# Kernel tuning notes

Hardware: AMD Instinct MI355X
Metric: run time of the kernel (lower is better)

The kernel has to match this reference:

```python
import jax, jax.numpy as jnp
from jax import lax
import numpy as np

DN = ('NCHW', 'OIHW', 'NCHW')

def conv_reflect(x, w, b, pad):
    # torch Conv2d with padding_mode='reflect': reflect-pad then valid conv
    x = jnp.pad(x, ((0, 0), (0, 0), (pad, pad), (pad, pad)), mode='reflect')
    y = lax.conv_general_dilated(x, w, (1, 1), 'VALID', dimension_numbers=DN)
    return y + b[None, :, None, None]

def setup_inputs() -> dict:
    key = jax.random.key(0)
    ks = jax.random.split(key, 8)
    B, W, H = 4, 1024, 1024
    inp = {
        'input': jax.random.normal(ks[0], (B, 12, W, H), dtype=jnp.float32),
        'w1': jax.random.normal(ks[1], (32, 12, 7, 7), dtype=jnp.float32) * 0.05,
        'b1': jnp.zeros((32,), dtype=jnp.float32),
        'w2': jax.random.normal(ks[2], (32, 32, 5, 5), dtype=jnp.float32) * 0.05,
        'b2': jnp.zeros((32,), dtype=jnp.float32),
        'w3': jax.random.normal(ks[3], (8, 32, 5, 5), dtype=jnp.float32) * 0.05,
        'b3': jnp.zeros((8,), dtype=jnp.float32),
        'dwkernel': jax.random.normal(ks[4], (8, 1, 7, 7), dtype=jnp.float32),
    }
    return inp

def reference(input, w1, b1, w2, b2, w3, b3, dwkernel):
    B, _, W, H = input.shape
    color = input[:, 0:3]
    albedo = input[:, 3:6]
    albedo = jnp.where(albedo < 0.001, jnp.float32(1.0), albedo)
    color = color / albedo
    net_in = jnp.concatenate([color, albedo, input[:, 6:]], axis=1)  # (B,12,W,H)

    h = jax.nn.relu(conv_reflect(net_in, w1, b1, 3))
    h = jax.nn.relu(conv_reflect(h, w2, b2, 2))
    logits = conv_reflect(h, w3, b3, 2)  # (B,8,W,H)
    kernel = jax.nn.softmax(logits / 5.0, axis=1)  # (B,8,W,H)

    # grouped conv: dwkernel repeated over 3 color channels, zero padding=3
    rpk = jnp.tile(dwkernel, (3, 1, 1, 1))  # (24,1,7,7)
    preconv = lax.conv_general_dilated(
        color, rpk, (1, 1), [(3, 3), (3, 3)],
        dimension_numbers=DN, feature_group_count=3,
    )  # (B,24,W,H)
    preconv = preconv.reshape(B, 3, 8, W, H)

    # (kernel expanded over color dim * preconv).sum over kernel dim
    filtered = jnp.einsum('bkwh,bckwh->bcwh', kernel, preconv)
    remodulated = albedo * filtered
    return remodulated
```

## Files before the change

kernel.cpp:

```cpp
#include <hip/hip_runtime.h>

#define IMG 1024

typedef _Float16 half8 __attribute__((ext_vector_type(8)));
typedef float f32x4 __attribute__((ext_vector_type(4)));

__device__ __forceinline__ int refl(int i) {
    i = (i < 0) ? -i : i;
    return (i >= IMG) ? (2 * IMG - 2 - i) : i;
}
__device__ __forceinline__ float afix(float a) { return (a < 0.001f) ? 1.0f : a; }
__device__ __forceinline__ int iclamp(int v, int lo, int hi) { return v < lo ? lo : (v > hi ? hi : v); }
__device__ __forceinline__ int swz64(int a) { return a ^ (((((a >> 6) & 3) ^ ((a >> 8) & 1)) << 4)); }
__device__ __forceinline__ int swz32(int a) { return a ^ ((((a >> 7) & 1)) << 4); }
__device__ __forceinline__ unsigned short h2b(_Float16 h) { union { _Float16 f; unsigned short u; } x; x.f = h; return x.u; }

__global__ void wprep_kernel(const float* __restrict__ w1, const float* __restrict__ w2,
                             const float* __restrict__ w3,
                             char* __restrict__ w1p, char* __restrict__ w2p, char* __restrict__ w3p)
{
    const int NF1 = 7 * 2 * 4 * 2, NF2 = 5 * 2 * 5 * 2, NF3 = 5 * 5 * 2;
    int gid = blockIdx.x * 256 + threadIdx.x;
    int f = gid >> 6, l = gid & 63;
    if (f >= NF1 + NF2 + NF3) return;
    int r = l & 15, g = l >> 4;
    half8 out;
    char* dst;
    if (f < NF1) {
        int pl = f & 1, j = (f >> 1) & 3, oct = (f >> 3) & 1, ky = f >> 4;
        int oc = oct * 16 + r;
#pragma unroll
        for (int e = 0; e < 8; e++) {
            int k = g * 8 + e, kx = 2 * j + (k >> 4), ic = k & 15;
            float v = (ic < 12 && kx < 7) ? w1[((oc * 12 + ic) * 7 + ky) * 7 + kx] : 0.f;
            _Float16 h = (_Float16)v;
            out[e] = pl ? (_Float16)(v - (float)h) : h;
        }
        dst = w1p + (size_t)f * 1024 + l * 16;
    } else if (f < NF1 + NF2) {
        int ff = f - NF1;
        int pl = ff & 1, t2 = ff >> 1;
        int kx = t2 % 5; t2 /= 5;
        int oct = t2 & 1, ky = t2 >> 1;
        int oc = oct * 16 + r;
#pragma unroll
        for (int e = 0; e < 8; e++) {
            int ic = g * 8 + e;
            float v = w2[((oc * 32 + ic) * 5 + ky) * 5 + kx];
            _Float16 h = (_Float16)v;
            out[e] = pl ? (_Float16)(v - (float)h) : h;
        }
        dst = w2p + (size_t)ff * 1024 + l * 16;
    } else {
        int ff = f - NF1 - NF2;
        int pl = ff & 1, t2 = ff >> 1;
        int kx = t2 % 5, ky = t2 / 5;
#pragma unroll
        for (int e = 0; e < 8; e++) {
            int ic = g * 8 + e;
            float v = (r < 8) ? w3[((r * 32 + ic) * 5 + ky) * 5 + kx] : 0.f;
            _Float16 h = (_Float16)v;
            out[e] = pl ? (_Float16)(v - (float)h) : h;
        }
        dst = w3p + (size_t)ff * 1024 + l * 16;
    }
    *(half8*)dst = out;
}

__global__ void netin_kernel(const float* __restrict__ in, char* __restrict__ nh, char* __restrict__ nl)
{
    const int M = IMG * IMG;
    int px = blockIdx.x * 256 + threadIdx.x;
    float v[16];
#pragma unroll
    for (int c = 0; c < 3; c++) {
        float a = afix(in[(size_t)(c + 3) * M + px]);
        v[c] = (in[(size_t)c * M + px] / a) * 0.25f;
        v[c + 3] = a * 0.25f;
    }
#pragma unroll
    for (int c = 6; c < 12; c++) v[c] = in[(size_t)c * M + px] * 0.25f;
#pragma unroll
    for (int c = 12; c < 16; c++) v[c] = 0.f;
    unsigned short hb[16], lb[16];
#pragma unroll
    for (int c = 0; c < 16; c++) {
        _Float16 h = (_Float16)v[c];
        hb[c] = h2b(h);
        lb[c] = h2b((_Float16)(v[c] - (float)h));
    }
    *(int4*)(nh + (size_t)px * 32) = *(int4*)&hb[0];
    *(int4*)(nh + (size_t)px * 32 + 16) = *(int4*)&hb[8];
    *(int4*)(nl + (size_t)px * 32) = *(int4*)&lb[0];
    *(int4*)(nl + (size_t)px * 32 + 16) = *(int4*)&lb[8];
}

__global__ __launch_bounds__(256, 4) void conv1_mfma(
    const char* __restrict__ nh, const char* __restrict__ nl,
    const char* __restrict__ w1p, const float* __restrict__ b1,
    char* __restrict__ h1h, char* __restrict__ h1l, int a1, int e1)
{
    __shared__ __align__(16) char sm[14 * 1280];
    const int t = threadIdx.x, l = t & 63, w = t >> 6;
    const int c = l & 15, g = l >> 4;
    const int x0 = blockIdx.x * 32;
    const int ystart = a1 + blockIdx.y * 8;
    const int pxt = w & 1, rbase = (w >> 1) * 4;

    f32x4 zero4 = {0.f, 0.f, 0.f, 0.f};
    f32x4 acc[2][4];
#pragma unroll
    for (int o = 0; o < 2; o++)
#pragma unroll
        for (int r = 0; r < 4; r++) acc[o][r] = zero4;

    for (int q = t; q < 1120; q += 256) {
        int slab = q / 80, c2 = q % 80;
        int px = c2 >> 1, s = c2 & 1;
        int gy = refl(ystart + slab - 3);
        int gx = refl(x0 + px - 3);
        *(int4*)(sm + slab * 1280 + swz32(px * 32 + s * 16)) =
            *(const int4*)(nh + ((size_t)gy * IMG + gx) * 32 + s * 16);
    }
    __syncthreads();
#pragma unroll 1
    for (int ky = 0; ky < 7; ky++) {
        half8 aw0[2][4], aw1[2][4];
#pragma unroll
        for (int oct = 0; oct < 2; oct++)
#pragma unroll
            for (int j = 0; j < 4; j++) {
                aw0[oct][j] = *(const half8*)(w1p + (size_t)((((ky * 2 + oct) * 4 + j) * 2 + 0)) * 1024 + l * 16);
                aw1[oct][j] = *(const half8*)(w1p + (size_t)((((ky * 2 + oct) * 4 + j) * 2 + 1)) * 1024 + l * 16);
            }
#pragma unroll
        for (int r = 0; r < 4; r++) {
            const char* base = sm + (rbase + r + ky) * 1280;
#pragma unroll
            for (int j = 0; j < 4; j++) {
                int p2 = pxt * 16 + c + 2 * j + (g >> 1);
                half8 bh = *(const half8*)(base + swz32(p2 * 32 + (g & 1) * 16));
#pragma unroll
                for (int oct = 0; oct < 2; oct++) {
                    acc[oct][r] = __builtin_amdgcn_mfma_f32_16x16x32_f16(aw0[oct][j], bh, acc[oct][r], 0, 0, 0);
                    acc[oct][r] = __builtin_amdgcn_mfma_f32_16x16x32_f16(aw1[oct][j], bh, acc[oct][r], 0, 0, 0);
                }
            }
        }
    }
    __syncthreads();
    for (int q = t; q < 1120; q += 256) {
        int slab = q / 80, c2 = q % 80;
        int px = c2 >> 1, s = c2 & 1;
        int gy = refl(ystart + slab - 3);
        int gx = refl(x0 + px - 3);
        *(int4*)(sm + slab * 1280 + swz32(px * 32 + s * 16)) =
            *(const int4*)(nl + ((size_t)gy * IMG + gx) * 32 + s * 16);
    }
    __syncthreads();
#pragma unroll 1
    for (int ky = 0; ky < 7; ky++) {
        half8 aw0[2][4];
#pragma unroll
        for (int oct = 0; oct < 2; oct++)
#pragma unroll
            for (int j = 0; j < 4; j++)
                aw0[oct][j] = *(const half8*)(w1p + (size_t)((((ky * 2 + oct) * 4 + j) * 2 + 0)) * 1024 + l * 16);
#pragma unroll
        for (int r = 0; r < 4; r++) {
            const char* base = sm + (rbase + r + ky) * 1280;
#pragma unroll
            for (int j = 0; j < 4; j++) {
                int p2 = pxt * 16 + c + 2 * j + (g >> 1);
                half8 bl = *(const half8*)(base + swz32(p2 * 32 + (g & 1) * 16));
#pragma unroll
                for (int oct = 0; oct < 2; oct++)
                    acc[oct][r] = __builtin_amdgcn_mfma_f32_16x16x32_f16(aw0[oct][j], bl, acc[oct][r], 0, 0, 0);
            }
        }
    }
#pragma unroll
    for (int r = 0; r < 4; r++) {
        int y = ystart + rbase + r;
        if (y < e1) {
            int x = x0 + pxt * 16 + c, ybuf = y - a1;
#pragma unroll
            for (int oct = 0; oct < 2; oct++) {
                ushort4 hv, lv;
                float vv[4];
#pragma unroll
                for (int i = 0; i < 4; i++) {
                    int oc = oct * 16 + g * 4 + i;
                    float v = acc[oct][r][i] * 4.f + b1[oc];
                    vv[i] = fmaxf(v, 0.f) * 0.125f;
                }
                _Float16 h0 = (_Float16)vv[0], h1_ = (_Float16)vv[1], h2_ = (_Float16)vv[2], h3 = (_Float16)vv[3];
                hv.x = h2b(h0); hv.y = h2b(h1_); hv.z = h2b(h2_); hv.w = h2b(h3);
                lv.x = h2b((_Float16)(vv[0] - (float)h0)); lv.y = h2b((_Float16)(vv[1] - (float)h1_));
                lv.z = h2b((_Float16)(vv[2] - (float)h2_)); lv.w = h2b((_Float16)(vv[3] - (float)h3));
                size_t ob = ((size_t)ybuf * IMG + x) * 64 + oct * 32 + g * 8;
                *(ushort4*)(h1h + ob) = hv;
                *(ushort4*)(h1l + ob) = lv;
            }
        }
    }
}

__global__ __launch_bounds__(256, 4) void conv2_mfma(
    const char* __restrict__ h1h, const char* __restrict__ h1l,
    const char* __restrict__ w2p, const float* __restrict__ b2,
    char* __restrict__ h2h, char* __restrict__ h2l,
    int a1, int e1, int a2, int e2)
{
    __shared__ __align__(16) char sm[12 * 2304];
    const int t = threadIdx.x, l = t & 63, w = t >> 6;
    const int c = l & 15, g = l >> 4;
    const int x0 = blockIdx.x * 32;
    const int ystart = a2 + blockIdx.y * 8;
    const int pxt = w & 1, rbase = (w >> 1) * 4;

    f32x4 zero4 = {0.f, 0.f, 0.f, 0.f};
    f32x4 acc[2][4];
#pragma unroll
    for (int o = 0; o < 2; o++)
#pragma unroll
        for (int r = 0; r < 4; r++) acc[o][r] = zero4;

    for (int q = t; q < 1728; q += 256) {
        int slab = q / 144, c2 = q % 144;
        int px = c2 >> 2, s = c2 & 3;
        int yy = iclamp(refl(ystart + slab - 2), a1, e1 - 1) - a1;
        int gx = refl(x0 + px - 2);
        *(int4*)(sm + slab * 2304 + swz64(px * 64 + s * 16)) =
            *(const int4*)(h1h + ((size_t)yy * IMG + gx) * 64 + s * 16);
    }
    __syncthreads();
#pragma unroll 1
    for (int ky = 0; ky < 5; ky++) {
        half8 aw0[2][5], aw1[2][5];
#pragma unroll
        for (int oct = 0; oct < 2; oct++)
#pragma unroll
            for (int kx = 0; kx < 5; kx++) {
                aw0[oct][kx] = *(const half8*)(w2p + (size_t)((((ky * 2 + oct) * 5 + kx) * 2 + 0)) * 1024 + l * 16);
                aw1[oct][kx] = *(const half8*)(w2p + (size_t)((((ky * 2 + oct) * 5 + kx) * 2 + 1)) * 1024 + l * 16);
            }
#pragma unroll
        for (int r = 0; r < 4; r++) {
            const char* base = sm + (rbase + r + ky) * 2304;
#pragma unroll
            for (int kx = 0; kx < 5; kx++) {
                half8 bh = *(const half8*)(base + swz64((pxt * 16 + c + kx) * 64 + g * 16));
#pragma unroll
                for (int oct = 0; oct < 2; oct++) {
                    acc[oct][r] = __builtin_amdgcn_mfma_f32_16x16x32_f16(aw0[oct][kx], bh, acc[oct][r], 0, 0, 0);
                    acc[oct][r] = __builtin_amdgcn_mfma_f32_16x16x32_f16(aw1[oct][kx], bh, acc[oct][r], 0, 0, 0);
                }
            }
        }
    }
    __syncthreads();
    for (int q = t; q < 1728; q += 256) {
        int slab = q / 144, c2 = q % 144;
        int px = c2 >> 2, s = c2 & 3;
        int yy = iclamp(refl(ystart + slab - 2), a1, e1 - 1) - a1;
        int gx = refl(x0 + px - 2);
        *(int4*)(sm + slab * 2304 + swz64(px * 64 + s * 16)) =
            *(const int4*)(h1l + ((size_t)yy * IMG + gx) * 64 + s * 16);
    }
    __syncthreads();
#pragma unroll 1
    for (int ky = 0; ky < 5; ky++) {
        half8 aw0[2][5];
#pragma unroll
        for (int oct = 0; oct < 2; oct++)
#pragma unroll
            for (int kx = 0; kx < 5; kx++)
                aw0[oct][kx] = *(const half8*)(w2p + (size_t)((((ky * 2 + oct) * 5 + kx) * 2 + 0)) * 1024 + l * 16);
#pragma unroll
        for (int r = 0; r < 4; r++) {
            const char* base = sm + (rbase + r + ky) * 2304;
#pragma unroll
            for (int kx = 0; kx < 5; kx++) {
                half8 bl = *(const half8*)(base + swz64((pxt * 16 + c + kx) * 64 + g * 16));
#pragma unroll
                for (int oct = 0; oct < 2; oct++)
                    acc[oct][r] = __builtin_amdgcn_mfma_f32_16x16x32_f16(aw0[oct][kx], bl, acc[oct][r], 0, 0, 0);
            }
        }
    }
#pragma unroll
    for (int r = 0; r < 4; r++) {
        int y = ystart + rbase + r;
        if (y < e2) {
            int x = x0 + pxt * 16 + c, ybuf = y - a2;
#pragma unroll
            for (int oct = 0; oct < 2; oct++) {
                ushort4 hv, lv;
                float vv[4];
#pragma unroll
                for (int i = 0; i < 4; i++) {
                    int oc = oct * 16 + g * 4 + i;
                    float v = acc[oct][r][i] * 8.f + b2[oc];
                    vv[i] = fmaxf(v, 0.f) * 0.125f;
                }
                _Float16 h0 = (_Float16)vv[0], h1_ = (_Float16)vv[1], h2_ = (_Float16)vv[2], h3 = (_Float16)vv[3];
                hv.x = h2b(h0); hv.y = h2b(h1_); hv.z = h2b(h2_); hv.w = h2b(h3);
                lv.x = h2b((_Float16)(vv[0] - (float)h0)); lv.y = h2b((_Float16)(vv[1] - (float)h1_));
                lv.z = h2b((_Float16)(vv[2] - (float)h2_)); lv.w = h2b((_Float16)(vv[3] - (float)h3));
                size_t ob = ((size_t)ybuf * IMG + x) * 64 + oct * 32 + g * 8;
                *(ushort4*)(h2h + ob) = hv;
                *(ushort4*)(h2l + ob) = lv;
            }
        }
    }
}

__global__ __launch_bounds__(256, 4) void conv3_mfma(
    const char* __restrict__ h2h, const char* __restrict__ h2l,
    const char* __restrict__ w3p, const float* __restrict__ b3,
    float* __restrict__ lg, int a2, int e2, int r0, int r1, int rowsL)
{
    __shared__ __align__(16) char sm[12 * 2304];
    const int t = threadIdx.x, l = t & 63, w = t >> 6;
    const int c = l & 15, g = l >> 4;
    const int x0 = blockIdx.x * 32;
    const int ystart = r0 + blockIdx.y * 8;
    const int pxt = w & 1, rbase = (w >> 1) * 4;

    f32x4 zero4 = {0.f, 0.f, 0.f, 0.f};
    f32x4 acc[4];
#pragma unroll
    for (int r = 0; r < 4; r++) acc[r] = zero4;

    for (int q = t; q < 1728; q += 256) {
        int slab = q / 144, c2 = q % 144;
        int px = c2 >> 2, s = c2 & 3;
        int yy = iclamp(refl(ystart + slab - 2), a2, e2 - 1) - a2;
        int gx = refl(x0 + px - 2);
        *(int4*)(sm + slab * 2304 + swz64(px * 64 + s * 16)) =
            *(const int4*)(h2h + ((size_t)yy * IMG + gx) * 64 + s * 16);
    }
    __syncthreads();
#pragma unroll 1
    for (int ky = 0; ky < 5; ky++) {
        half8 aw0[5], aw1[5];
#pragma unroll
        for (int kx = 0; kx < 5; kx++) {
            aw0[kx] = *(const half8*)(w3p + (size_t)(((ky * 5 + kx) * 2 + 0)) * 1024 + l * 16);
            aw1[kx] = *(const half8*)(w3p + (size_t)(((ky * 5 + kx) * 2 + 1)) * 1024 + l * 16);
        }
#pragma unroll
        for (int r = 0; r < 4; r++) {
            const char* base = sm + (rbase + r + ky) * 2304;
#pragma unroll
            for (int kx = 0; kx < 5; kx++) {
                half8 bh = *(const half8*)(base + swz64((pxt * 16 + c + kx) * 64 + g * 16));
                acc[r] = __builtin_amdgcn_mfma_f32_16x16x32_f16(aw0[kx], bh, acc[r], 0, 0, 0);
                acc[r] = __builtin_amdgcn_mfma_f32_16x16x32_f16(aw1[kx], bh, acc[r], 0, 0, 0);
            }
        }
    }
    __syncthreads();
    for (int q = t; q < 1728; q += 256) {
        int slab = q / 144, c2 = q % 144;
        int px = c2 >> 2, s = c2 & 3;
        int yy = iclamp(refl(ystart + slab - 2), a2, e2 - 1) - a2;
        int gx = refl(x0 + px - 2);
        *(int4*)(sm + slab * 2304 + swz64(px * 64 + s * 16)) =
            *(const int4*)(h2l + ((size_t)yy * IMG + gx) * 64 + s * 16);
    }
    __syncthreads();
#pragma unroll 1
    for (int ky = 0; ky < 5; ky++) {
        half8 aw0[5];
#pragma unroll
        for (int kx = 0; kx < 5; kx++)
            aw0[kx] = *(const half8*)(w3p + (size_t)(((ky * 5 + kx) * 2 + 0)) * 1024 + l * 16);
#pragma unroll
        for (int r = 0; r < 4; r++) {
            const char* base = sm + (rbase + r + ky) * 2304;
#pragma unroll
            for (int kx = 0; kx < 5; kx++) {
                half8 bl = *(const half8*)(base + swz64((pxt * 16 + c + kx) * 64 + g * 16));
                acc[r] = __builtin_amdgcn_mfma_f32_16x16x32_f16(aw0[kx], bl, acc[r], 0, 0, 0);
            }
        }
    }
#pragma unroll
    for (int r = 0; r < 4; r++) {
        int y = ystart + rbase + r;
        if (y < r1 && g < 2) {
            int x = x0 + pxt * 16 + c, row = y - r0;
#pragma unroll
            for (int i = 0; i < 4; i++) {
                int oc = g * 4 + i;
                lg[((size_t)oc * rowsL + row) * IMG + x] = acc[r][i] * 8.f + b3[oc];
            }
        }
    }
}

__global__ __launch_bounds__(256, 2) void final_kernel(
    const float* __restrict__ in, const float* __restrict__ lg, const float* __restrict__ dw,
    float* __restrict__ outp, int ylo, int yhi, int rowsL)
{
    __shared__ __align__(16) float sC[3][22][72];
    __shared__ __align__(16) float sdw[8][49];
    const int t = threadIdx.x;
    const int tx = t & 15, ty = t >> 4;
    const int x0 = blockIdx.x * 64;
    const int y0 = ylo + blockIdx.y * 16;

    for (int e = t; e < 8 * 49; e += 256) sdw[e / 49][e % 49] = dw[e];
    for (int e = t; e < 3 * 22 * 70; e += 256) {
        int c = e / (22 * 70), rem = e % (22 * 70);
        int r = rem / 70, cc = rem % 70;
        int gy = y0 + r - 3, gx = x0 + cc - 3;
        float v = 0.f;
        if (gy >= 0 && gy < IMG && gx >= 0 && gx < IMG) {
            float a = afix(in[(size_t)(c + 3) * IMG * IMG + (size_t)gy * IMG + gx]);
            v = in[(size_t)c * IMG * IMG + (size_t)gy * IMG + gx] / a;
        }
        sC[c][r][cc] = v;
    }
    __syncthreads();
    const int y = y0 + ty;
    if (y >= yhi) return;

    float lv[4][8];
#pragma unroll
    for (int k = 0; k < 8; k++) {
        float4 v = *(const float4*)&lg[((size_t)k * rowsL + (y - ylo)) * IMG + x0 + tx * 4];
        lv[0][k] = v.x; lv[1][k] = v.y; lv[2][k] = v.z; lv[3][k] = v.w;
    }
    float p[4][8];
#pragma unroll
    for (int j = 0; j < 4; j++) {
        float m = -3.4e38f;
#pragma unroll
        for (int k = 0; k < 8; k++) m = fmaxf(m, lv[j][k]);
        float s = 0.f;
#pragma unroll
        for (int k = 0; k < 8; k++) { float ev = __expf((lv[j][k] - m) * 0.2f); p[j][k] = ev; s += ev; }
        float invs = 1.0f / s;
#pragma unroll
        for (int k = 0; k < 8; k++) p[j][k] *= invs;
    }

    float filt[3][4];
#pragma unroll
    for (int c = 0; c < 3; c++)
#pragma unroll
        for (int j = 0; j < 4; j++) filt[c][j] = 0.f;

#pragma unroll 1
    for (int ky = 0; ky < 7; ky++) {
        float cv[3][10];
#pragma unroll
        for (int c = 0; c < 3; c++)
#pragma unroll
            for (int jj = 0; jj < 10; jj++) cv[c][jj] = sC[c][ty + ky][tx * 4 + jj];
#pragma unroll
        for (int kx = 0; kx < 7; kx++) {
            float dwv[8];
#pragma unroll
            for (int k = 0; k < 8; k++) dwv[k] = sdw[k][ky * 7 + kx];
#pragma unroll
            for (int j = 0; j < 4; j++) {
                float e0 = 0.f;
#pragma unroll
                for (int k = 0; k < 8; k++) e0 = fmaf(p[j][k], dwv[k], e0);
#pragma unroll
                for (int c = 0; c < 3; c++) filt[c][j] = fmaf(e0, cv[c][kx + j], filt[c][j]);
            }
        }
    }
#pragma unroll
    for (int c = 0; c < 3; c++) {
        const float* ap = &in[(size_t)(c + 3) * IMG * IMG + (size_t)y * IMG + x0 + tx * 4];
        float4 a4 = *(const float4*)ap;
        float4 o4 = make_float4(afix(a4.x) * filt[c][0], afix(a4.y) * filt[c][1],
                                afix(a4.z) * filt[c][2], afix(a4.w) * filt[c][3]);
        *(float4*)&outp[(size_t)c * IMG * IMG + (size_t)y * IMG + x0 + tx * 4] = o4;
    }
}

extern "C" void kernel_launch(void* const* d_in, const int* in_sizes, int n_in,
                              void* d_out, int out_size, void* d_ws, size_t ws_size,
                              hipStream_t stream)
{
    const float* in  = (const float*)d_in[0];
    const float* w1  = (const float*)d_in[1];
    const float* b1  = (const float*)d_in[2];
    const float* w2  = (const float*)d_in[3];
    const float* b2  = (const float*)d_in[4];
    const float* w3  = (const float*)d_in[5];
    const float* b3  = (const float*)d_in[6];
    const float* dw  = (const float*)d_in[7];
    float* out = (float*)d_out;

    const size_t WB1 = 112 * 1024, WB2 = 100 * 1024, WB3 = 50 * 1024;
    const size_t NETIN = (size_t)IMG * IMG * 32;

    int S = 1024;
    while (S > 64) {
        size_t need = WB1 + WB2 + WB3 + 2 * NETIN
                    + 2ull * (S + 8) * IMG * 64 + 2ull * (S + 4) * IMG * 64
                    + (size_t)S * IMG * 8 * 4;
        if (need <= ws_size) break;
        S >>= 1;
    }
    const int rows1 = S + 8, rows2 = S + 4, rowsL = S;

    char* w1p = (char*)d_ws;
    char* w2p = w1p + WB1;
    char* w3p = w2p + WB2;
    char* nh  = w3p + WB3;
    char* nl  = nh + NETIN;
    char* h1h = nl + NETIN;
    char* h1l = h1h + (size_t)rows1 * IMG * 64;
    char* h2h = h1l + (size_t)rows1 * IMG * 64;
    char* h2l = h2h + (size_t)rows2 * IMG * 64;
    float* lgb = (float*)(h2l + (size_t)rows2 * IMG * 64);

    wprep_kernel<<<66, 256, 0, stream>>>(w1, w2, w3, w1p, w2p, w3p);

    for (int b = 0; b < 4; b++) {
        const float* inb = in + (size_t)b * 12 * IMG * IMG;
        float* outb = out + (size_t)b * 3 * IMG * IMG;
        netin_kernel<<<IMG * IMG / 256, 256, 0, stream>>>(inb, nh, nl);
        for (int r0 = 0; r0 < IMG; r0 += S) {
            int r1 = r0 + S; if (r1 > IMG) r1 = IMG;
            int a1 = r0 - 4; if (a1 < 0) a1 = 0;
            int e1 = r1 + 4; if (e1 > IMG) e1 = IMG;
            int a2 = r0 - 2; if (a2 < 0) a2 = 0;
            int e2 = r1 + 2; if (e2 > IMG) e2 = IMG;
            conv1_mfma<<<dim3(32, (e1 - a1 + 7) / 8), 256, 0, stream>>>(nh, nl, w1p, b1, h1h, h1l, a1, e1);
            conv2_mfma<<<dim3(32, (e2 - a2 + 7) / 8), 256, 0, stream>>>(h1h, h1l, w2p, b2, h2h, h2l, a1, e1, a2, e2);
            conv3_mfma<<<dim3(32, (r1 - r0 + 7) / 8), 256, 0, stream>>>(h2h, h2l, w3p, b3, lgb, a2, e2, r0, r1, rowsL);
            final_kernel<<<dim3(16, (r1 - r0 + 15) / 16), 256, 0, stream>>>(inb, lgb, dw, outb, r0, r1, rowsL);
        }
    }
}
```

Measured before the change: 1.994 ms.

## Switch conv1/conv2 to 32x32x16 MFMA with kx-outer row-reuse loop

Conv1 and conv2 now use 32x32x16 MFMA tiles (32 output channels by 32 pixels per wave) with 128-thread blocks, and the weight packing is reordered to match. All three convs use a restructured loop that loads each LDS row once per kx and applies it to every output row it contributes to. A fast path skips reflect and clamp index math on interior tiles. The aim is fewer LDS reads and less instruction overhead per MFMA. In exchange there are more accumulator registers, fewer waves per block, and weights are read from global/cache inside the inner loop instead of from preloaded registers.

```diff
diff --git a/kernel.cpp b/kernel.cpp
--- a/kernel.cpp
+++ b/kernel.cpp
@@ -4,6 +4,7 @@
 
 typedef _Float16 half8 __attribute__((ext_vector_type(8)));
 typedef float f32x4 __attribute__((ext_vector_type(4)));
+typedef float f32x16 __attribute__((ext_vector_type(16)));
 
 __device__ __forceinline__ int refl(int i) {
     i = (i < 0) ? -i : i;
@@ -19,46 +20,49 @@
                              const float* __restrict__ w3,
                              char* __restrict__ w1p, char* __restrict__ w2p, char* __restrict__ w3p)
 {
-    const int NF1 = 7 * 2 * 4 * 2, NF2 = 5 * 2 * 5 * 2, NF3 = 5 * 5 * 2;
+    const int NF1 = 98, NF2 = 100, NF3 = 50;
     int gid = blockIdx.x * 256 + threadIdx.x;
     int f = gid >> 6, l = gid & 63;
     if (f >= NF1 + NF2 + NF3) return;
-    int r = l & 15, g = l >> 4;
     half8 out;
     char* dst;
     if (f < NF1) {
-        int pl = f & 1, j = (f >> 1) & 3, oct = (f >> 3) & 1, ky = f >> 4;
-        int oc = oct * 16 + r;
+        int pl = f & 1, kk = f >> 1;
+        int kx = kk % 7, ky = kk / 7;
+        int oc = l & 31;
 #pragma unroll
         for (int e = 0; e < 8; e++) {
-            int k = g * 8 + e, kx = 2 * j + (k >> 4), ic = k & 15;
-            float v = (ic < 12 && kx < 7) ? w1[((oc * 12 + ic) * 7 + ky) * 7 + kx] : 0.f;
+            int ii = (l >> 5) * 8 + e;
+            float v = (ii < 12) ? w1[((oc * 12 + ii) * 7 + ky) * 7 + kx] : 0.f;
             _Float16 h = (_Float16)v;
             out[e] = pl ? (_Float16)(v - (float)h) : h;
         }
         dst = w1p + (size_t)f * 1024 + l * 16;
     } else if (f < NF1 + NF2) {
         int ff = f - NF1;
-        int pl = ff & 1, t2 = ff >> 1;
-        int kx = t2 % 5; t2 /= 5;
-        int oct = t2 & 1, ky = t2 >> 1;
-        int oc = oct * 16 + r;
+        int pl = ff & 1, kh = (ff >> 1) & 1, kk = ff >> 2;
+        int kx = kk % 5, ky = kk / 5;
+        int oc = l & 31;
 #pragma unroll
         for (int e = 0; e < 8; e++) {
-            int ic = g * 8 + e;
-            float v = w2[((oc * 32 + ic) * 5 + ky) * 5 + kx];
+            int i = (l >> 5) * 8 + e;
+            int ch = (i & 3) + 8 * (i >> 2) + 4 * kh;
+            float v = w2[((oc * 32 + ch) * 5 + ky) * 5 + kx];
             _Float16 h = (_Float16)v;
             out[e] = pl ? (_Float16)(v - (float)h) : h;
         }
         dst = w2p + (size_t)ff * 1024 + l * 16;
     } else {
         int ff = f - NF1 - NF2;
-        int pl = ff & 1, t2 = ff >> 1;
-        int kx = t2 % 5, ky = t2 / 5;
+        int pl = ff & 1, kk = ff >> 1;
+        int kx = kk % 5, ky = kk / 5;
+        int r = l & 15;
 #pragma unroll
         for (int e = 0; e < 8; e++) {
-            int ic = g * 8 + e;
-            float v = (r < 8) ? w3[((r * 32 + ic) * 5 + ky) * 5 + kx] : 0.f;
+            int q = (l >> 4) * 8 + e;
+            int i = q & 15, hl = q >> 4;
+            int ch = (i & 3) + 8 * (i >> 2) + 4 * hl;
+            float v = (r < 8) ? w3[((r * 32 + ch) * 5 + ky) * 5 + kx] : 0.f;
             _Float16 h = (_Float16)v;
             out[e] = pl ? (_Float16)(v - (float)h) : h;
         }
@@ -95,118 +99,138 @@
     *(int4*)(nl + (size_t)px * 32 + 16) = *(int4*)&lb[8];
 }
 
-__global__ __launch_bounds__(256, 4) void conv1_mfma(
+__device__ __forceinline__ void conv1_compute(const char* sm, const char* __restrict__ w1p,
+                                              f32x16 acc[4], int l, int rbase, bool two)
+{
+    const int px = l & 31, hl = l >> 5;
+#pragma unroll 1
+    for (int kx = 0; kx < 7; kx++) {
+        const int off = swz32((kx + px) * 32 + hl * 16);
+#pragma unroll
+        for (int s = 0; s < 10; s++) {
+            half8 b = *(const half8*)(sm + (rbase + s) * 1280 + off);
+#pragma unroll
+            for (int ky = 0; ky < 7; ky++) {
+                const int r = s - ky;
+                if (r >= 0 && r < 4) {
+                    const char* wb = w1p + (size_t)((ky * 7 + kx) * 2) * 1024 + l * 16;
+                    acc[r] = __builtin_amdgcn_mfma_f32_32x32x16_f16(*(const half8*)wb, b, acc[r], 0, 0, 0);
+                    if (two)
+                        acc[r] = __builtin_amdgcn_mfma_f32_32x32x16_f16(*(const half8*)(wb + 1024), b, acc[r], 0, 0, 0);
+                }
+            }
+        }
+    }
+}
+
+__global__ __launch_bounds__(128, 2) void conv1_mfma(
     const char* __restrict__ nh, const char* __restrict__ nl,
     const char* __restrict__ w1p, const float* __restrict__ b1,
     char* __restrict__ h1h, char* __restrict__ h1l, int a1, int e1)
 {
     __shared__ __align__(16) char sm[14 * 1280];
     const int t = threadIdx.x, l = t & 63, w = t >> 6;
-    const int c = l & 15, g = l >> 4;
+    const int px = l & 31, hl = l >> 5;
     const int x0 = blockIdx.x * 32;
     const int ystart = a1 + blockIdx.y * 8;
-    const int pxt = w & 1, rbase = (w >> 1) * 4;
-
-    f32x4 zero4 = {0.f, 0.f, 0.f, 0.f};
-    f32x4 acc[2][4];
-#pragma unroll
-    for (int o = 0; o < 2; o++)
-#pragma unroll
-        for (int r = 0; r < 4; r++) acc[o][r] = zero4;
-
-    for (int q = t; q < 1120; q += 256) {
-        int slab = q / 80, c2 = q % 80;
-        int px = c2 >> 1, s = c2 & 1;
-        int gy = refl(ystart + slab - 3);
-        int gx = refl(x0 + px - 3);
-        *(int4*)(sm + slab * 1280 + swz32(px * 32 + s * 16)) =
-            *(const int4*)(nh + ((size_t)gy * IMG + gx) * 32 + s * 16);
-    }
-    __syncthreads();
-#pragma unroll 1
-    for (int ky = 0; ky < 7; ky++) {
-        half8 aw0[2][4], aw1[2][4];
-#pragma unroll
-        for (int oct = 0; oct < 2; oct++)
-#pragma unroll
-            for (int j = 0; j < 4; j++) {
-                aw0[oct][j] = *(const half8*)(w1p + (size_t)((((ky * 2 + oct) * 4 + j) * 2 + 0)) * 1024 + l * 16);
-                aw1[oct][j] = *(const half8*)(w1p + (size_t)((((ky * 2 + oct) * 4 + j) * 2 + 1)) * 1024 + l * 16);
-            }
-#pragma unroll
-        for (int r = 0; r < 4; r++) {
-            const char* base = sm + (rbase + r + ky) * 1280;
-#pragma unroll
-            for (int j = 0; j < 4; j++) {
-                int p2 = pxt * 16 + c + 2 * j + (g >> 1);
-                half8 bh = *(const half8*)(base + swz32(p2 * 32 + (g & 1) * 16));
-#pragma unroll
-                for (int oct = 0; oct < 2; oct++) {
-                    acc[oct][r] = __builtin_amdgcn_mfma_f32_16x16x32_f16(aw0[oct][j], bh, acc[oct][r], 0, 0, 0);
-                    acc[oct][r] = __builtin_amdgcn_mfma_f32_16x16x32_f16(aw1[oct][j], bh, acc[oct][r], 0, 0, 0);
-                }
-            }
-        }
-    }
-    __syncthreads();
-    for (int q = t; q < 1120; q += 256) {
-        int slab = q / 80, c2 = q % 80;
-        int px = c2 >> 1, s = c2 & 1;
-        int gy = refl(ystart + slab - 3);
-        int gx = refl(x0 + px - 3);
-        *(int4*)(sm + slab * 1280 + swz32(px * 32 + s * 16)) =
-            *(const int4*)(nl + ((size_t)gy * IMG + gx) * 32 + s * 16);
-    }
-    __syncthreads();
-#pragma unroll 1
-    for (int ky = 0; ky < 7; ky++) {
-        half8 aw0[2][4];
-#pragma unroll
-        for (int oct = 0; oct < 2; oct++)
-#pragma unroll
-            for (int j = 0; j < 4; j++)
-                aw0[oct][j] = *(const half8*)(w1p + (size_t)((((ky * 2 + oct) * 4 + j) * 2 + 0)) * 1024 + l * 16);
-#pragma unroll
-        for (int r = 0; r < 4; r++) {
-            const char* base = sm + (rbase + r + ky) * 1280;
-#pragma unroll
-            for (int j = 0; j < 4; j++) {
-                int p2 = pxt * 16 + c + 2 * j + (g >> 1);
-                half8 bl = *(const half8*)(base + swz32(p2 * 32 + (g & 1) * 16));
-#pragma unroll
-                for (int oct = 0; oct < 2; oct++)
-                    acc[oct][r] = __builtin_amdgcn_mfma_f32_16x16x32_f16(aw0[oct][j], bl, acc[oct][r], 0, 0, 0);
-            }
-        }
-    }
+    const int rbase = w * 4;
+    const bool fast = (x0 >= 3) && (x0 + 37 <= IMG) && (ystart >= 3) && (ystart + 11 <= IMG);
+
+    f32x16 acc[4];
+#pragma unroll
+    for (int r = 0; r < 4; r++)
+#pragma unroll
+        for (int i = 0; i < 16; i++) acc[r][i] = 0.f;
+
+    if (fast) {
+        const char* rb = nh + ((size_t)(ystart - 3) * IMG + (x0 - 3)) * 32;
+        for (int q = t; q < 1120; q += 128) {
+            int slab = q / 80, c2 = q % 80;
+            *(int4*)(sm + slab * 1280 + swz32(c2 * 16)) = *(const int4*)(rb + (size_t)slab * (IMG * 32) + c2 * 16);
+        }
+    } else {
+        for (int q = t; q < 1120; q += 128) {
+            int slab = q / 80, c2 = q % 80;
+            int gy = refl(ystart + slab - 3), gx = refl(x0 + (c2 >> 1) - 3);
+            *(int4*)(sm + slab * 1280 + swz32(c2 * 16)) =
+                *(const int4*)(nh + ((size_t)gy * IMG + gx) * 32 + (c2 & 1) * 16);
+        }
+    }
+    __syncthreads();
+    conv1_compute(sm, w1p, acc, l, rbase, true);
+    __syncthreads();
+    if (fast) {
+        const char* rb = nl + ((size_t)(ystart - 3) * IMG + (x0 - 3)) * 32;
+        for (int q = t; q < 1120; q += 128) {
+            int slab = q / 80, c2 = q % 80;
+            *(int4*)(sm + slab * 1280 + swz32(c2 * 16)) = *(const int4*)(rb + (size_t)slab * (IMG * 32) + c2 * 16);
+        }
+    } else {
+        for (int q = t; q < 1120; q += 128) {
+            int slab = q / 80, c2 = q % 80;
+            int gy = refl(ystart + slab - 3), gx = refl(x0 + (c2 >> 1) - 3);
+            *(int4*)(sm + slab * 1280 + swz32(c2 * 16)) =
+                *(const int4*)(nl + ((size_t)gy * IMG + gx) * 32 + (c2 & 1) * 16);
+        }
+    }
+    __syncthreads();
+    conv1_compute(sm, w1p, acc, l, rbase, false);
+
 #pragma unroll
     for (int r = 0; r < 4; r++) {
         int y = ystart + rbase + r;
         if (y < e1) {
-            int x = x0 + pxt * 16 + c, ybuf = y - a1;
-#pragma unroll
-            for (int oct = 0; oct < 2; oct++) {
-                ushort4 hv, lv;
-                float vv[4];
-#pragma unroll
-                for (int i = 0; i < 4; i++) {
-                    int oc = oct * 16 + g * 4 + i;
-                    float v = acc[oct][r][i] * 4.f + b1[oc];
-                    vv[i] = fmaxf(v, 0.f) * 0.125f;
+            int x = x0 + px, ybuf = y - a1;
+            unsigned short hb[16], lb[16];
+#pragma unroll
+            for (int i = 0; i < 16; i++) {
+                int oc = (i & 3) + 8 * (i >> 2) + 4 * hl;
+                float v = acc[r][i] * 4.f + b1[oc];
+                v = fmaxf(v, 0.f) * 0.125f;
+                _Float16 h = (_Float16)v;
+                hb[i] = h2b(h);
+                lb[i] = h2b((_Float16)(v - (float)h));
+            }
+            size_t ob = ((size_t)ybuf * IMG + x) * 64 + hl * 32;
+            *(int4*)(h1h + ob) = *(int4*)&hb[0];
+            *(int4*)(h1h + ob + 16) = *(int4*)&hb[8];
+            *(int4*)(h1l + ob) = *(int4*)&lb[0];
+            *(int4*)(h1l + ob + 16) = *(int4*)&lb[8];
+        }
+    }
+}
+
+__device__ __forceinline__ void conv2_compute(const char* sm, const char* __restrict__ wp,
+                                              f32x16 acc[4], int l, int rbase, bool two)
+{
+    const int px = l & 31, hl = l >> 5;
+#pragma unroll 1
+    for (int kx = 0; kx < 5; kx++) {
+        const int off0 = swz64((kx + px) * 64 + hl * 16);
+        const int off1 = swz64((kx + px) * 64 + 32 + hl * 16);
+#pragma unroll
+        for (int s = 0; s < 8; s++) {
+            const char* sl = sm + (rbase + s) * 2304;
+            half8 bk0 = *(const half8*)(sl + off0);
+            half8 bk1 = *(const half8*)(sl + off1);
+#pragma unroll
+            for (int ky = 0; ky < 5; ky++) {
+                const int r = s - ky;
+                if (r >= 0 && r < 4) {
+                    const char* wb = wp + (size_t)((ky * 5 + kx) * 4) * 1024 + l * 16;
+                    acc[r] = __builtin_amdgcn_mfma_f32_32x32x16_f16(*(const half8*)wb, bk0, acc[r], 0, 0, 0);
+                    if (two)
+                        acc[r] = __builtin_amdgcn_mfma_f32_32x32x16_f16(*(const half8*)(wb + 1024), bk0, acc[r], 0, 0, 0);
+                    acc[r] = __builtin_amdgcn_mfma_f32_32x32x16_f16(*(const half8*)(wb + 2048), bk1, acc[r], 0, 0, 0);
+                    if (two)
+                        acc[r] = __builtin_amdgcn_mfma_f32_32x32x16_f16(*(const half8*)(wb + 3072), bk1, acc[r], 0, 0, 0);
                 }
-                _Float16 h0 = (_Float16)vv[0], h1_ = (_Float16)vv[1], h2_ = (_Float16)vv[2], h3 = (_Float16)vv[3];
-                hv.x = h2b(h0); hv.y = h2b(h1_); hv.z = h2b(h2_); hv.w = h2b(h3);
-                lv.x = h2b((_Float16)(vv[0] - (float)h0)); lv.y = h2b((_Float16)(vv[1] - (float)h1_));
-                lv.z = h2b((_Float16)(vv[2] - (float)h2_)); lv.w = h2b((_Float16)(vv[3] - (float)h3));
-                size_t ob = ((size_t)ybuf * IMG + x) * 64 + oct * 32 + g * 8;
-                *(ushort4*)(h1h + ob) = hv;
-                *(ushort4*)(h1l + ob) = lv;
-            }
-        }
-    }
-}
-
-__global__ __launch_bounds__(256, 4) void conv2_mfma(
+            }
+        }
+    }
+}
+
+__global__ __launch_bounds__(128, 2) void conv2_mfma(
     const char* __restrict__ h1h, const char* __restrict__ h1l,
     const char* __restrict__ w2p, const float* __restrict__ b2,
     char* __restrict__ h2h, char* __restrict__ h2l,
@@ -214,103 +238,97 @@
 {
     __shared__ __align__(16) char sm[12 * 2304];
     const int t = threadIdx.x, l = t & 63, w = t >> 6;
-    const int c = l & 15, g = l >> 4;
+    const int px = l & 31, hl = l >> 5;
     const int x0 = blockIdx.x * 32;
     const int ystart = a2 + blockIdx.y * 8;
-    const int pxt = w & 1, rbase = (w >> 1) * 4;
-
-    f32x4 zero4 = {0.f, 0.f, 0.f, 0.f};
-    f32x4 acc[2][4];
-#pragma unroll
-    for (int o = 0; o < 2; o++)
-#pragma unroll
-        for (int r = 0; r < 4; r++) acc[o][r] = zero4;
-
-    for (int q = t; q < 1728; q += 256) {
-        int slab = q / 144, c2 = q % 144;
-        int px = c2 >> 2, s = c2 & 3;
-        int yy = iclamp(refl(ystart + slab - 2), a1, e1 - 1) - a1;
-        int gx = refl(x0 + px - 2);
-        *(int4*)(sm + slab * 2304 + swz64(px * 64 + s * 16)) =
-            *(const int4*)(h1h + ((size_t)yy * IMG + gx) * 64 + s * 16);
-    }
-    __syncthreads();
-#pragma unroll 1
-    for (int ky = 0; ky < 5; ky++) {
-        half8 aw0[2][5], aw1[2][5];
-#pragma unroll
-        for (int oct = 0; oct < 2; oct++)
-#pragma unroll
-            for (int kx = 0; kx < 5; kx++) {
-                aw0[oct][kx] = *(const half8*)(w2p + (size_t)((((ky * 2 + oct) * 5 + kx) * 2 + 0)) * 1024 + l * 16);
-                aw1[oct][kx] = *(const half8*)(w2p + (size_t)((((ky * 2 + oct) * 5 + kx) * 2 + 1)) * 1024 + l * 16);
-            }
-#pragma unroll
-        for (int r = 0; r < 4; r++) {
-            const char* base = sm + (rbase + r + ky) * 2304;
-#pragma unroll
-            for (int kx = 0; kx < 5; kx++) {
-                half8 bh = *(const half8*)(base + swz64((pxt * 16 + c + kx) * 64 + g * 16));
-#pragma unroll
-                for (int oct = 0; oct < 2; oct++) {
-                    acc[oct][r] = __builtin_amdgcn_mfma_f32_16x16x32_f16(aw0[oct][kx], bh, acc[oct][r], 0, 0, 0);
-                    acc[oct][r] = __builtin_amdgcn_mfma_f32_16x16x32_f16(aw1[oct][kx], bh, acc[oct][r], 0, 0, 0);
-                }
-            }
-        }
-    }
-    __syncthreads();
-    for (int q = t; q < 1728; q += 256) {
-        int slab = q / 144, c2 = q % 144;
-        int px = c2 >> 2, s = c2 & 3;
-        int yy = iclamp(refl(ystart + slab - 2), a1, e1 - 1) - a1;
-        int gx = refl(x0 + px - 2);
-        *(int4*)(sm + slab * 2304 + swz64(px * 64 + s * 16)) =
-            *(const int4*)(h1l + ((size_t)yy * IMG + gx) * 64 + s * 16);
-    }
-    __syncthreads();
-#pragma unroll 1
-    for (int ky = 0; ky < 5; ky++) {
-        half8 aw0[2][5];
-#pragma unroll
-        for (int oct = 0; oct < 2; oct++)
-#pragma unroll
-            for (int kx = 0; kx < 5; kx++)
-                aw0[oct][kx] = *(const half8*)(w2p + (size_t)((((ky * 2 + oct) * 5 + kx) * 2 + 0)) * 1024 + l * 16);
-#pragma unroll
-        for (int r = 0; r < 4; r++) {
-            const char* base = sm + (rbase + r + ky) * 2304;
-#pragma unroll
-            for (int kx = 0; kx < 5; kx++) {
-                half8 bl = *(const half8*)(base + swz64((pxt * 16 + c + kx) * 64 + g * 16));
-#pragma unroll
-                for (int oct = 0; oct < 2; oct++)
-                    acc[oct][r] = __builtin_amdgcn_mfma_f32_16x16x32_f16(aw0[oct][kx], bl, acc[oct][r], 0, 0, 0);
-            }
-        }
-    }
+    const int rbase = w * 4;
+    const bool fast = (x0 >= 2) && (x0 + 34 <= IMG) && (ystart - 2 >= a1) && (ystart + 10 <= e1);
+
+    f32x16 acc[4];
+#pragma unroll
+    for (int r = 0; r < 4; r++)
+#pragma unroll
+        for (int i = 0; i < 16; i++) acc[r][i] = 0.f;
+
+    if (fast) {
+        const char* rb = h1h + (((size_t)(ystart - 2 - a1)) * IMG + (x0 - 2)) * 64;
+        for (int q = t; q < 1728; q += 128) {
+            int slab = q / 144, c2 = q % 144;
+            *(int4*)(sm + slab * 2304 + swz64(c2 * 16)) = *(const int4*)(rb + (size_t)slab * (IMG * 64) + c2 * 16);
+        }
+    } else {
+        for (int q = t; q < 1728; q += 128) {
+            int slab = q / 144, c2 = q % 144;
+            int yy = iclamp(refl(ystart + slab - 2), a1, e1 - 1) - a1;
+            int gx = refl(x0 + (c2 >> 2) - 2);
+            *(int4*)(sm + slab * 2304 + swz64(c2 * 16)) =
+                *(const int4*)(h1h + ((size_t)yy * IMG + gx) * 64 + (c2 & 3) * 16);
+        }
+    }
+    __syncthreads();
+    conv2_compute(sm, w2p, acc, l, rbase, true);
+    __syncthreads();
+    if (fast) {
+        const char* rb = h1l + (((size_t)(ystart - 2 - a1)) * IMG + (x0 - 2)) * 64;
+        for (int q = t; q < 1728; q += 128) {
+            int slab = q / 144, c2 = q % 144;
+            *(int4*)(sm + slab * 2304 + swz64(c2 * 16)) = *(const int4*)(rb + (size_t)slab * (IMG * 64) + c2 * 16);
+        }
+    } else {
+        for (int q = t; q < 1728; q += 128) {
+            int slab = q / 144, c2 = q % 144;
+            int yy = iclamp(refl(ystart + slab - 2), a1, e1 - 1) - a1;
+            int gx = refl(x0 + (c2 >> 2) - 2);
+            *(int4*)(sm + slab * 2304 + swz64(c2 * 16)) =
+                *(const int4*)(h1l + ((size_t)yy * IMG + gx) * 64 + (c2 & 3) * 16);
+        }
+    }
+    __syncthreads();
+    conv2_compute(sm, w2p, acc, l, rbase, false);
+
 #pragma unroll
     for (int r = 0; r < 4; r++) {
         int y = ystart + rbase + r;
         if (y < e2) {
-            int x = x0 + pxt * 16 + c, ybuf = y - a2;
-#pragma unroll
-            for (int oct = 0; oct < 2; oct++) {
-                ushort4 hv, lv;
-                float vv[4];
-#pragma unroll
-                for (int i = 0; i < 4; i++) {
-                    int oc = oct * 16 + g * 4 + i;
-                    float v = acc[oct][r][i] * 8.f + b2[oc];
-                    vv[i] = fmaxf(v, 0.f) * 0.125f;
+            int x = x0 + px, ybuf = y - a2;
+            unsigned short hb[16], lb[16];
+#pragma unroll
+            for (int i = 0; i < 16; i++) {
+                int oc = (i & 3) + 8 * (i >> 2) + 4 * hl;
+                float v = acc[r][i] * 8.f + b2[oc];
+                v = fmaxf(v, 0.f) * 0.125f;
+                _Float16 h = (_Float16)v;
+                hb[i] = h2b(h);
+                lb[i] = h2b((_Float16)(v - (float)h));
+            }
+            size_t ob = ((size_t)ybuf * IMG + x) * 64 + hl * 32;
+            *(int4*)(h2h + ob) = *(int4*)&hb[0];
+            *(int4*)(h2h + ob + 16) = *(int4*)&hb[8];
+            *(int4*)(h2l + ob) = *(int4*)&lb[0];
+            *(int4*)(h2l + ob + 16) = *(int4*)&lb[8];
+        }
+    }
+}
+
+__device__ __forceinline__ void conv3_compute(const char* sm, const char* __restrict__ wp,
+                                              f32x4 acc[4], int l, int pxt, int rbase, bool two)
+{
+    const int c = l & 15, g = l >> 4;
+#pragma unroll 1
+    for (int kx = 0; kx < 5; kx++) {
+        const int off = swz64((pxt * 16 + c + kx) * 64 + g * 16);
+#pragma unroll
+        for (int s = 0; s < 8; s++) {
+            half8 b = *(const half8*)(sm + (rbase + s) * 2304 + off);
+#pragma unroll
+            for (int ky = 0; ky < 5; ky++) {
+                const int r = s - ky;
+                if (r >= 0 && r < 4) {
+                    const char* wb = wp + (size_t)((ky * 5 + kx) * 2) * 1024 + l * 16;
+                    acc[r] = __builtin_amdgcn_mfma_f32_16x16x32_f16(*(const half8*)wb, b, acc[r], 0, 0, 0);
+                    if (two)
+                        acc[r] = __builtin_amdgcn_mfma_f32_16x16x32_f16(*(const half8*)(wb + 1024), b, acc[r], 0, 0, 0);
                 }
-                _Float16 h0 = (_Float16)vv[0], h1_ = (_Float16)vv[1], h2_ = (_Float16)vv[2], h3 = (_Float16)vv[3];
-                hv.x = h2b(h0); hv.y = h2b(h1_); hv.z = h2b(h2_); hv.w = h2b(h3);
-                lv.x = h2b((_Float16)(vv[0] - (float)h0)); lv.y = h2b((_Float16)(vv[1] - (float)h1_));
-                lv.z = h2b((_Float16)(vv[2] - (float)h2_)); lv.w = h2b((_Float16)(vv[3] - (float)h3));
-                size_t ob = ((size_t)ybuf * IMG + x) * 64 + oct * 32 + g * 8;
-                *(ushort4*)(h2h + ob) = hv;
-                *(ushort4*)(h2l + ob) = lv;
             }
         }
     }
@@ -327,66 +345,48 @@
     const int x0 = blockIdx.x * 32;
     const int ystart = r0 + blockIdx.y * 8;
     const int pxt = w & 1, rbase = (w >> 1) * 4;
-
-    f32x4 zero4 = {0.f, 0.f, 0.f, 0.f};
+    const bool fast = (x0 >= 2) && (x0 + 34 <= IMG) && (ystart - 2 >= a2) && (ystart + 10 <= e2);
+
     f32x4 acc[4];
 #pragma unroll
-    for (int r = 0; r < 4; r++) acc[r] = zero4;
-
-    for (int q = t; q < 1728; q += 256) {
-        int slab = q / 144, c2 = q % 144;
-        int px = c2 >> 2, s = c2 & 3;
-        int yy = iclamp(refl(ystart + slab - 2), a2, e2 - 1) - a2;
-        int gx = refl(x0 + px - 2);
-        *(int4*)(sm + slab * 2304 + swz64(px * 64 + s * 16)) =
-            *(const int4*)(h2h + ((size_t)yy * IMG + gx) * 64 + s * 16);
-    }
-    __syncthreads();
-#pragma unroll 1
-    for (int ky = 0; ky < 5; ky++) {
-        half8 aw0[5], aw1[5];
-#pragma unroll
-        for (int kx = 0; kx < 5; kx++) {
-            aw0[kx] = *(const half8*)(w3p + (size_t)(((ky * 5 + kx) * 2 + 0)) * 1024 + l * 16);
-            aw1[kx] = *(const half8*)(w3p + (size_t)(((ky * 5 + kx) * 2 + 1)) * 1024 + l * 16);
-        }
-#pragma unroll
-        for (int r = 0; r < 4; r++) {
-            const char* base = sm + (rbase + r + ky) * 2304;
-#pragma unroll
-            for (int kx = 0; kx < 5; kx++) {
-                half8 bh = *(const half8*)(base + swz64((pxt * 16 + c + kx) * 64 + g * 16));
-                acc[r] = __builtin_amdgcn_mfma_f32_16x16x32_f16(aw0[kx], bh, acc[r], 0, 0, 0);
-                acc[r] = __builtin_amdgcn_mfma_f32_16x16x32_f16(aw1[kx], bh, acc[r], 0, 0, 0);
-            }
-        }
-    }
-    __syncthreads();
-    for (int q = t; q < 1728; q += 256) {
-        int slab = q / 144, c2 = q % 144;
-        int px = c2 >> 2, s = c2 & 3;
-        int yy = iclamp(refl(ystart + slab - 2), a2, e2 - 1) - a2;
-        int gx = refl(x0 + px - 2);
-        *(int4*)(sm + slab * 2304 + swz64(px * 64 + s * 16)) =
-            *(const int4*)(h2l + ((size_t)yy * IMG + gx) * 64 + s * 16);
-    }
-    __syncthreads();
-#pragma unroll 1
-    for (int ky = 0; ky < 5; ky++) {
-        half8 aw0[5];
-#pragma unroll
-        for (int kx = 0; kx < 5; kx++)
-            aw0[kx] = *(const half8*)(w3p + (size_t)(((ky * 5 + kx) * 2 + 0)) * 1024 + l * 16);
-#pragma unroll
-        for (int r = 0; r < 4; r++) {
-            const char* base = sm + (rbase + r + ky) * 2304;
-#pragma unroll
-            for (int kx = 0; kx < 5; kx++) {
-                half8 bl = *(const half8*)(base + swz64((pxt * 16 + c + kx) * 64 + g * 16));
-                acc[r] = __builtin_amdgcn_mfma_f32_16x16x32_f16(aw0[kx], bl, acc[r], 0, 0, 0);
-            }
-        }
-    }
+    for (int r = 0; r < 4; r++) { acc[r][0] = 0.f; acc[r][1] = 0.f; acc[r][2] = 0.f; acc[r][3] = 0.f; }
+
+    if (fast) {
+        const char* rb = h2h + (((size_t)(ystart - 2 - a2)) * IMG + (x0 - 2)) * 64;
+        for (int q = t; q < 1728; q += 256) {
+            int slab = q / 144, c2 = q % 144;
+            *(int4*)(sm + slab * 2304 + swz64(c2 * 16)) = *(const int4*)(rb + (size_t)slab * (IMG * 64) + c2 * 16);
+        }
+    } else {
+        for (int q = t; q < 1728; q += 256) {
+            int slab = q / 144, c2 = q % 144;
+            int yy = iclamp(refl(ystart + slab - 2), a2, e2 - 1) - a2;
+            int gx = refl(x0 + (c2 >> 2) - 2);
+            *(int4*)(sm + slab * 2304 + swz64(c2 * 16)) =
+                *(const int4*)(h2h + ((size_t)yy * IMG + gx) * 64 + (c2 & 3) * 16);
+        }
+    }
+    __syncthreads();
+    conv3_compute(sm, w3p, acc, l, pxt, rbase, true);
+    __syncthreads();
+    if (fast) {
+        const char* rb = h2l + (((size_t)(ystart - 2 - a2)) * IMG + (x0 - 2)) * 64;
+        for (int q = t; q < 1728; q += 256) {
+            int slab = q / 144, c2 = q % 144;
+            *(int4*)(sm + slab * 2304 + swz64(c2 * 16)) = *(const int4*)(rb + (size_t)slab * (IMG * 64) + c2 * 16);
+        }
+    } else {
+        for (int q = t; q < 1728; q += 256) {
+            int slab = q / 144, c2 = q % 144;
+            int yy = iclamp(refl(ystart + slab - 2), a2, e2 - 1) - a2;
+            int gx = refl(x0 + (c2 >> 2) - 2);
+            *(int4*)(sm + slab * 2304 + swz64(c2 * 16)) =
+                *(const int4*)(h2l + ((size_t)yy * IMG + gx) * 64 + (c2 & 3) * 16);
+        }
+    }
+    __syncthreads();
+    conv3_compute(sm, w3p, acc, l, pxt, rbase, false);
+
 #pragma unroll
     for (int r = 0; r < 4; r++) {
         int y = ystart + rbase + r;
@@ -500,7 +500,7 @@
     const float* dw  = (const float*)d_in[7];
     float* out = (float*)d_out;
 
-    const size_t WB1 = 112 * 1024, WB2 = 100 * 1024, WB3 = 50 * 1024;
+    const size_t WB1 = 98 * 1024, WB2 = 100 * 1024, WB3 = 50 * 1024;
     const size_t NETIN = (size_t)IMG * IMG * 32;
 
     int S = 1024;
@@ -524,7 +524,7 @@
     char* h2l = h2h + (size_t)rows2 * IMG * 64;
     float* lgb = (float*)(h2l + (size_t)rows2 * IMG * 64);
 
-    wprep_kernel<<<66, 256, 0, stream>>>(w1, w2, w3, w1p, w2p, w3p);
+    wprep_kernel<<<62, 256, 0, stream>>>(w1, w2, w3, w1p, w2p, w3p);
 
     for (int b = 0; b < 4; b++) {
         const float* inb = in + (size_t)b * 12 * IMG * IMG;
@@ -536,8 +536,8 @@
             int e1 = r1 + 4; if (e1 > IMG) e1 = IMG;
             int a2 = r0 - 2; if (a2 < 0) a2 = 0;
             int e2 = r1 + 2; if (e2 > IMG) e2 = IMG;
-            conv1_mfma<<<dim3(32, (e1 - a1 + 7) / 8), 256, 0, stream>>>(nh, nl, w1p, b1, h1h, h1l, a1, e1);
-            conv2_mfma<<<dim3(32, (e2 - a2 + 7) / 8), 256, 0, stream>>>(h1h, h1l, w2p, b2, h2h, h2l, a1, e1, a2, e2);
+            conv1_mfma<<<dim3(32, (e1 - a1 + 7) / 8), 128, 0, stream>>>(nh, nl, w1p, b1, h1h, h1l, a1, e1);
+            conv2_mfma<<<dim3(32, (e2 - a2 + 7) / 8), 128, 0, stream>>>(h1h, h1l, w2p, b2, h2h, h2l, a1, e1, a2, e2);
             conv3_mfma<<<dim3(32, (r1 - r0 + 7) / 8), 256, 0, stream>>>(h2h, h2l, w3p, b3, lgb, a2, e2, r0, r1, rowsL);
             final_kernel<<<dim3(16, (r1 - r0 + 15) / 16), 256, 0, stream>>>(inb, lgb, dw, outb, r0, r1, rowsL);
         }
```

Result: slower. 2.065 ms (+3.5%).
